# Optimization experiments

Hardware: AMD Instinct MI355X
Metric: run time of the kernel (lower is better)

## Reference

```python
import jax, jax.numpy as jnp
import numpy as np

M, K, N, GROUP = 32, 8192, 28672, 128


def setup_inputs() -> dict:
    key = jax.random.key(0)
    k1, k2, k3, k4 = jax.random.split(key, 4)
    x = jax.random.normal(k1, (M, K), dtype=jnp.float16)
    # int32 words, each packing 8 consecutive int4 values along K
    qweight = jax.random.randint(k2, (K // 8, N), 0, 2147483647, dtype=jnp.int32)
    scales = (jax.random.uniform(k3, (K // GROUP, N), dtype=jnp.float32) * 0.01 + 0.001).astype(jnp.float16)
    bias = (jax.random.normal(k4, (N,), dtype=jnp.float32) * 0.02).astype(jnp.float16)
    return {"x": x, "qweight": qweight, "scales": scales, "bias": bias}


def reference(x, qweight, scales, bias):
    # Unpack 8 int4 nibbles per int32 word along K: (K//8, N) -> (K, N)
    K8, n = qweight.shape
    shifts = (jnp.arange(8, dtype=jnp.int32) * 4)[None, :, None]
    wq = ((qweight[:, None, :] >> shifts) & 15).reshape(K8 * 8, n)  # [K, N] in [0,15]
    # Dequant: zero-point fixed at 8 (pack() asserts zeros==8), per-group scales
    w = wq.astype(jnp.float16) - jnp.float16(8.0)
    g, gs = scales.shape[0], (K8 * 8) // scales.shape[0]
    w = (w.reshape(g, gs, n) * scales[:, None, :]).reshape(K8 * 8, n)  # [K, N] fp16
    return jnp.dot(x, w) + bias  # [M, N]
```

## Files before the change

kernel.cpp:

```cpp
#include <hip/hip_runtime.h>
#include <stdint.h>

#define K_DIM 8192
#define N_DIM 28672
#define NCT   (N_DIM / 128)

typedef _Float16 half8 __attribute__((ext_vector_type(8)));
typedef _Float16 half2t __attribute__((ext_vector_type(2)));
typedef float f32x16 __attribute__((ext_vector_type(16)));

__global__ __launch_bounds__(256) void prep_x(const float* __restrict__ x,
                                              _Float16* __restrict__ xp) {
  int idx = blockIdx.x * 256 + threadIdx.x;
  int m  = idx & 31;
  int k8 = idx >> 5;
  const float* p = x + (size_t)m * K_DIM + (size_t)k8 * 8;
  float4 xa = *(const float4*)p;
  float4 xb = *(const float4*)(p + 4);
  half2t p0 = __builtin_bit_cast(half2t, __builtin_amdgcn_cvt_pkrtz(xa.x, xb.x));
  half2t p1 = __builtin_bit_cast(half2t, __builtin_amdgcn_cvt_pkrtz(xa.y, xb.y));
  half2t p2 = __builtin_bit_cast(half2t, __builtin_amdgcn_cvt_pkrtz(xa.z, xb.z));
  half2t p3 = __builtin_bit_cast(half2t, __builtin_amdgcn_cvt_pkrtz(xa.w, xb.w));
  half8 o;
  o[0] = p0[0]; o[1] = p0[1]; o[2] = p1[0]; o[3] = p1[1];
  o[4] = p2[0]; o[5] = p2[1]; o[6] = p3[0]; o[7] = p3[1];
  *(half8*)(xp + ((size_t)k8 * 32 + m) * 8) = o;
}

__global__ __launch_bounds__(256) void zero_out(float4* __restrict__ out) {
  out[(size_t)blockIdx.x * 256 + threadIdx.x] = float4{0.f, 0.f, 0.f, 0.f};
}

static __device__ __forceinline__ half8 dqs(uint32_t w, half2t sh) {
  const uint32_t M4 = 0x000F000Fu, E = 0x64006400u;
  half2t off; off[0] = (_Float16)(-1032.0f); off[1] = (_Float16)(-1032.0f);
  half2t v0 = (__builtin_bit_cast(half2t, ( w        & M4) | E) + off) * sh;
  half2t v1 = (__builtin_bit_cast(half2t, ((w >> 4)  & M4) | E) + off) * sh;
  half2t v2 = (__builtin_bit_cast(half2t, ((w >> 8)  & M4) | E) + off) * sh;
  half2t v3 = (__builtin_bit_cast(half2t, ((w >> 12) & M4) | E) + off) * sh;
  half8 r;
  r[0] = v0[0]; r[1] = v0[1]; r[2] = v1[0]; r[3] = v1[1];
  r[4] = v2[0]; r[5] = v2[1]; r[6] = v3[0]; r[7] = v3[1];
  return r;
}

static __device__ __forceinline__ void gl_lds16(const void* g, void* l) {
  __builtin_amdgcn_global_load_lds(
      (const __attribute__((address_space(1))) uint32_t*)g,
      (__attribute__((address_space(3))) uint32_t*)l, 16, 0, 0);
}

static __device__ __forceinline__ void waitcnt_vm10() { __builtin_amdgcn_s_waitcnt(0x0F7A); }
static __device__ __forceinline__ void waitcnt_vm0()  { __builtin_amdgcn_s_waitcnt(0x0F70); }

__global__ __launch_bounds__(256, 4) void qgemm(
    const uint32_t* __restrict__ q, const float* __restrict__ scales,
    const float* __restrict__ bias, const _Float16* __restrict__ xp,
    float* __restrict__ out) {
  __shared__ __attribute__((aligned(16))) char smem[3 * 8192];
  const int tid  = threadIdx.x;
  const int w    = tid >> 6;
  const int lane = tid & 63;
  const int h    = lane >> 5;
  const int nl   = lane & 31;
  const int bid  = blockIdx.x;
  const int kblk = bid / NCT;
  const int ct   = bid - kblk * NCT;
  const int col0 = ct << 7;
  const int wr0  = kblk << 7;
  const int colw = col0 + (w << 5);

  half2t sh[8];
#pragma unroll
  for (int g = 0; g < 8; g++) {
    float s = scales[(size_t)(kblk * 8 + g) * N_DIM + colw + nl];
    sh[g] = __builtin_bit_cast(half2t, __builtin_amdgcn_cvt_pkrtz(s, s));
  }
  __builtin_amdgcn_sched_barrier(0);

  const uint64_t sb = (uint64_t)(uintptr_t)q +
                      ((uint64_t)wr0 * N_DIM + (uint64_t)col0) * 4u;
  const uint32_t vbase = (uint32_t)(((h * N_DIM) + (w << 5) + nl) * 4);
  const char* xb = (const char*)xp;

  uint32_t qr[3][8];

  auto qload = [&](int gg) {
#pragma unroll
    for (int i = 0; i < 8; i++) {
      uint32_t vo = vbase + (uint32_t)(8 * gg + i) * (uint32_t)(2 * N_DIM * 4);
      asm volatile("global_load_dword %0, %1, %2"
                   : "=v"(qr[gg % 3][i])
                   : "v"(vo), "s"(sb));
    }
  };
  auto stageA = [&](int gg) {
    char* A = smem + (gg % 3) * 8192;
    size_t ga = (size_t)(wr0 + 16 * gg) * 512 + (size_t)w * 2048 + (size_t)lane * 16;
#pragma unroll
    for (int j = 0; j < 2; j++)
      gl_lds16(xb + ga + j * 1024, A + w * 2048 + j * 1024);
  };

  f32x16 acc;
#pragma unroll
  for (int j = 0; j < 16; j++) acc[j] = 0.0f;

  qload(0); stageA(0); qload(1); stageA(1);

#pragma unroll
  for (int g = 0; g < 8; g++) {
    if (g < 7) waitcnt_vm10(); else waitcnt_vm0();
    __builtin_amdgcn_s_barrier();
    __builtin_amdgcn_sched_barrier(0);
    if (g + 2 < 8) { qload(g + 2); stageA(g + 2); }
    const char* A = smem + (g % 3) * 8192;
    half2t s = sh[g];
#pragma unroll
    for (int i = 0; i < 8; i++) {
      half8 af = *(const half8*)(A + ((2 * i + h) * 32 + nl) * 16);
      acc = __builtin_amdgcn_mfma_f32_32x32x16_f16(af, dqs(qr[g % 3][i], s),
                                                   acc, 0, 0, 0);
    }
  }

  float bs = (kblk == 0) ? bias[colw + nl] : 0.0f;
#pragma unroll
  for (int j = 0; j < 16; j++) {
    int row = (j & 3) + ((j >> 2) << 3) + (h << 2);
    unsafeAtomicAdd(&out[(size_t)row * N_DIM + colw + nl], acc[j] + bs);
  }
}

extern "C" void kernel_launch(void* const* d_in, const int* in_sizes, int n_in,
                              void* d_out, int out_size, void* d_ws, size_t ws_size,
                              hipStream_t stream) {
  const float*    xf      = (const float*)d_in[0];
  const uint32_t* qweight = (const uint32_t*)d_in[1];
  const float*    scales  = (const float*)d_in[2];
  const float*    bias    = (const float*)d_in[3];
  float*          out     = (float*)d_out;
  _Float16*       xp      = (_Float16*)d_ws;

  zero_out<<<dim3(896), dim3(256), 0, stream>>>((float4*)out);
  prep_x<<<dim3(128), dim3(256), 0, stream>>>(xf, xp);
  qgemm<<<dim3(NCT * 8), dim3(256), 0, stream>>>(qweight, scales, bias, xp, out);
}
```

Measured before the change: 187.4 us.

## Replace split-K atomics with per-block full-K reduction over 32 columns

Each block now owns 32 output columns and covers the full K, with its four waves splitting K and combining partial sums through an LDS reduction before a plain store. This removes the zero-fill kernel and the atomic adds to the output. Activations are loaded straight into registers with a double-buffered prefetch instead of being staged through LDS, so there are no per-group barriers. The grid shrinks to 896 blocks, which may cost occupancy, and every block now rereads the whole activation matrix.

```diff
diff --git a/kernel.cpp b/kernel.cpp
--- a/kernel.cpp
+++ b/kernel.cpp
@@ -3,7 +3,7 @@
 
 #define K_DIM 8192
 #define N_DIM 28672
-#define NCT   (N_DIM / 128)
+#define NG    16
 
 typedef _Float16 half8 __attribute__((ext_vector_type(8)));
 typedef _Float16 half2t __attribute__((ext_vector_type(2)));
@@ -27,10 +27,6 @@
   *(half8*)(xp + ((size_t)k8 * 32 + m) * 8) = o;
 }
 
-__global__ __launch_bounds__(256) void zero_out(float4* __restrict__ out) {
-  out[(size_t)blockIdx.x * 256 + threadIdx.x] = float4{0.f, 0.f, 0.f, 0.f};
-}
-
 static __device__ __forceinline__ half8 dqs(uint32_t w, half2t sh) {
   const uint32_t M4 = 0x000F000Fu, E = 0x64006400u;
   half2t off; off[0] = (_Float16)(-1032.0f); off[1] = (_Float16)(-1032.0f);
@@ -44,91 +40,91 @@
   return r;
 }
 
-static __device__ __forceinline__ void gl_lds16(const void* g, void* l) {
-  __builtin_amdgcn_global_load_lds(
-      (const __attribute__((address_space(1))) uint32_t*)g,
-      (__attribute__((address_space(3))) uint32_t*)l, 16, 0, 0);
-}
-
-static __device__ __forceinline__ void waitcnt_vm10() { __builtin_amdgcn_s_waitcnt(0x0F7A); }
-static __device__ __forceinline__ void waitcnt_vm0()  { __builtin_amdgcn_s_waitcnt(0x0F70); }
+static __device__ __forceinline__ void waitcnt_vm8() { __builtin_amdgcn_s_waitcnt(0x0F78); }
+static __device__ __forceinline__ void waitcnt_vm0() { __builtin_amdgcn_s_waitcnt(0x0F70); }
 
 __global__ __launch_bounds__(256, 4) void qgemm(
     const uint32_t* __restrict__ q, const float* __restrict__ scales,
     const float* __restrict__ bias, const _Float16* __restrict__ xp,
     float* __restrict__ out) {
-  __shared__ __attribute__((aligned(16))) char smem[3 * 8192];
+  __shared__ float red[4][16][64];
   const int tid  = threadIdx.x;
   const int w    = tid >> 6;
   const int lane = tid & 63;
   const int h    = lane >> 5;
   const int nl   = lane & 31;
-  const int bid  = blockIdx.x;
-  const int kblk = bid / NCT;
-  const int ct   = bid - kblk * NCT;
-  const int col0 = ct << 7;
-  const int wr0  = kblk << 7;
-  const int colw = col0 + (w << 5);
+  const int ct   = blockIdx.x;
+  const int c0   = ct << 5;
+  const int wr0  = w << 8;
 
-  half2t sh[8];
-#pragma unroll
-  for (int g = 0; g < 8; g++) {
-    float s = scales[(size_t)(kblk * 8 + g) * N_DIM + colw + nl];
-    sh[g] = __builtin_bit_cast(half2t, __builtin_amdgcn_cvt_pkrtz(s, s));
-  }
-  __builtin_amdgcn_sched_barrier(0);
+  const uint32_t qb  = (uint32_t)((((uint64_t)(wr0 + h)) * N_DIM + c0 + nl) * 4);
+  const uint32_t ab  = (uint32_t)(((wr0 + h) * 32 + nl) * 16);
+  const uint32_t sb  = (uint32_t)((((uint64_t)(w * NG)) * N_DIM + c0 + nl) * 4);
 
-  const uint64_t sb = (uint64_t)(uintptr_t)q +
-                      ((uint64_t)wr0 * N_DIM + (uint64_t)col0) * 4u;
-  const uint32_t vbase = (uint32_t)(((h * N_DIM) + (w << 5) + nl) * 4);
-  const char* xb = (const char*)xp;
+  uint32_t qr[2][8];
+  float4   aA[2][8];
+  uint32_t sv[2];
 
-  uint32_t qr[3][8];
-
-  auto qload = [&](int gg) {
+  auto qload = [&](int g, int p) {
 #pragma unroll
     for (int i = 0; i < 8; i++) {
-      uint32_t vo = vbase + (uint32_t)(8 * gg + i) * (uint32_t)(2 * N_DIM * 4);
+      uint32_t vo = qb + (uint32_t)(g * 16 + 2 * i) * (uint32_t)(N_DIM * 4);
       asm volatile("global_load_dword %0, %1, %2"
-                   : "=v"(qr[gg % 3][i])
-                   : "v"(vo), "s"(sb));
+                   : "=v"(qr[p][i]) : "v"(vo), "s"(q));
     }
   };
-  auto stageA = [&](int gg) {
-    char* A = smem + (gg % 3) * 8192;
-    size_t ga = (size_t)(wr0 + 16 * gg) * 512 + (size_t)w * 2048 + (size_t)lane * 16;
+  auto aload = [&](int g, int p) {
 #pragma unroll
-    for (int j = 0; j < 2; j++)
-      gl_lds16(xb + ga + j * 1024, A + w * 2048 + j * 1024);
+    for (int i = 0; i < 8; i++) {
+      uint32_t vo = ab + (uint32_t)(g * 8192 + i * 1024);
+      asm volatile("global_load_dwordx4 %0, %1, %2"
+                   : "=v"(aA[p][i]) : "v"(vo), "s"(xp));
+    }
+  };
+  auto sload = [&](int g, int p) {
+    uint32_t vo = sb + (uint32_t)g * (uint32_t)(N_DIM * 4);
+    asm volatile("global_load_dword %0, %1, %2"
+                 : "=v"(sv[p]) : "v"(vo), "s"(scales));
   };
 
   f32x16 acc;
 #pragma unroll
   for (int j = 0; j < 16; j++) acc[j] = 0.0f;
 
-  qload(0); stageA(0); qload(1); stageA(1);
+  qload(0, 0); sload(0, 0); aload(0, 0); qload(1, 1);
+
+  auto step = [&](int g, int p) {
+    if (g == NG - 1) waitcnt_vm0(); else waitcnt_vm8();
+    __builtin_amdgcn_sched_barrier(0);
+    float sf = __builtin_bit_cast(float, sv[p]);
+    half2t s2 = __builtin_bit_cast(half2t, __builtin_amdgcn_cvt_pkrtz(sf, sf));
+#pragma unroll
+    for (int i = 0; i < 8; i++) {
+      acc = __builtin_amdgcn_mfma_f32_32x32x16_f16(
+          __builtin_bit_cast(half8, aA[p][i]), dqs(qr[p][i], s2), acc, 0, 0, 0);
+    }
+    if (g + 1 < NG) { sload(g + 1, p ^ 1); aload(g + 1, p ^ 1); }
+    if (g + 2 < NG) qload(g + 2, p);
+  };
+
+#pragma unroll 2
+  for (int gg = 0; gg < NG; gg += 2) {
+    step(gg, 0);
+    step(gg + 1, 1);
+  }
 
 #pragma unroll
-  for (int g = 0; g < 8; g++) {
-    if (g < 7) waitcnt_vm10(); else waitcnt_vm0();
-    __builtin_amdgcn_s_barrier();
-    __builtin_amdgcn_sched_barrier(0);
-    if (g + 2 < 8) { qload(g + 2); stageA(g + 2); }
-    const char* A = smem + (g % 3) * 8192;
-    half2t s = sh[g];
+  for (int j = 0; j < 16; j++) red[w][j][lane] = acc[j];
+  __syncthreads();
+
+  float b = bias[c0 + nl];
 #pragma unroll
-    for (int i = 0; i < 8; i++) {
-      half8 af = *(const half8*)(A + ((2 * i + h) * 32 + nl) * 16);
-      acc = __builtin_amdgcn_mfma_f32_32x32x16_f16(af, dqs(qr[g % 3][i], s),
-                                                   acc, 0, 0, 0);
-    }
-  }
-
-  float bs = (kblk == 0) ? bias[colw + nl] : 0.0f;
-#pragma unroll
-  for (int j = 0; j < 16; j++) {
+  for (int jj = 0; jj < 4; jj++) {
+    int j = w * 4 + jj;
+    float v = red[0][j][lane] + red[1][j][lane] +
+              red[2][j][lane] + red[3][j][lane];
     int row = (j & 3) + ((j >> 2) << 3) + (h << 2);
-    unsafeAtomicAdd(&out[(size_t)row * N_DIM + colw + nl], acc[j] + bs);
+    out[(size_t)row * N_DIM + c0 + nl] = v + b;
   }
 }
 
@@ -142,7 +138,6 @@
   float*          out     = (float*)d_out;
   _Float16*       xp      = (_Float16*)d_ws;
 
-  zero_out<<<dim3(896), dim3(256), 0, stream>>>((float4*)out);
   prep_x<<<dim3(128), dim3(256), 0, stream>>>(xf, xp);
-  qgemm<<<dim3(NCT * 8), dim3(256), 0, stream>>>(qweight, scales, bias, xp, out);
+  qgemm<<<dim3(N_DIM / 32), dim3(256), 0, stream>>>(qweight, scales, bias, xp, out);
 }
```

After: 208.8 us. 11.4% more time.
